# Performance work log

Hardware: AMD Instinct MI355X
Metric: run time of the kernel (lower is better)

Reference implementation:

```python
import jax, jax.numpy as jnp
import numpy as np

N_NODES = 51200
N_EDGES = 614400
ORIG = 92
AFL = 64      # atom_fea_len
NFL = 64      # nbr_fea_len
BINS = 100
N_CONV = 3
EPS = 1e-5


def _bn(h, g, b):
    # BatchNorm1d in training mode: biased batch statistics over dim 0
    mu = h.mean(0)
    var = h.var(0)
    return (h - mu) * jax.lax.rsqrt(var + EPS) * g + b


def setup_inputs() -> dict:
    key = jax.random.key(0)
    ks = jax.random.split(key, 16)
    inp = {
        "x": jax.random.normal(ks[0], (N_NODES, ORIG), dtype=jnp.float32),
        "edge_index": jax.random.randint(ks[1], (2, N_EDGES), 0, N_NODES, dtype=jnp.int32),
        "edge_attr": jax.random.uniform(ks[2], (N_EDGES, 1), dtype=jnp.float32),
        "batchsize": 128,
        # encoder-level params
        "attention": jnp.ones((ORIG,), jnp.float32),
        "emb_W": jax.random.normal(ks[3], (ORIG, AFL), jnp.float32) / np.sqrt(ORIG),
        "emb_b": jnp.zeros((AFL,), jnp.float32),
        # per-conv params stacked along axis 0 (n_conv layers)
        "ad_w1": jax.random.normal(ks[4], (N_CONV, 1, BINS), jnp.float32),
        "ad_b1": jnp.zeros((N_CONV, BINS), jnp.float32),
        "ad_w2": jax.random.normal(ks[5], (N_CONV, BINS, BINS), jnp.float32) / np.sqrt(BINS),
        "ad_b2": jnp.zeros((N_CONV, BINS), jnp.float32),
        "ad_alpha": jax.random.uniform(ks[6], (N_CONV, 1), dtype=jnp.float32),
        "ad_lut": jax.random.uniform(ks[7], (N_CONV, BINS, NFL), dtype=jnp.float32),
        "fc_W": jax.random.normal(ks[8], (N_CONV, 2 * AFL + NFL, 2 * AFL), jnp.float32) / np.sqrt(2 * AFL + NFL),
        "fc_b": jnp.zeros((N_CONV, 2 * AFL), jnp.float32),
        "bn1_g": jnp.ones((N_CONV, 2 * AFL), jnp.float32),
        "bn1_b": jnp.zeros((N_CONV, 2 * AFL), jnp.float32),
        "bn2_g": jnp.ones((N_CONV, AFL), jnp.float32),
        "bn2_b": jnp.zeros((N_CONV, AFL), jnp.float32),
        # pre_pooling linear
        "pp_W": jax.random.normal(ks[9], (AFL, AFL), jnp.float32) / np.sqrt(AFL),
        "pp_b": jnp.zeros((AFL,), jnp.float32),
    }
    return inp


def _cgconv(h, src, dst, edge_attr, w1, b1, w2, b2, alpha, lut, fcW, fcb, g1, be1, g2, be2):
    # AutoDiscretization of the scalar edge feature -> [E, NFL]
    v2 = jax.nn.leaky_relu(edge_attr @ w1 + b1)               # [E, BINS]
    v3 = v2 @ w2 + b2 + alpha * v2                            # [E, BINS]
    e = jax.nn.softmax(v3, axis=-1) @ lut                     # [E, NFL]
    # message: gather endpoints, fused gated MLP (x_i = target, x_j = source)
    z = jnp.concatenate([h[dst], h[src], e], axis=1) @ fcW + fcb  # [E, 2*AFL]
    z = _bn(z, g1, be1)
    nbr_filter, nbr_core = jnp.split(z, 2, axis=1)
    msg = jax.nn.relu(nbr_filter) * jax.nn.relu(nbr_core)     # [E, AFL]
    # aggregate (scatter-add to target nodes) + update
    aggr = jax.ops.segment_sum(msg, dst, num_segments=N_NODES)
    return jax.nn.relu(h + _bn(aggr, g2, be2))


def reference(x, edge_index, edge_attr, batchsize, attention, emb_W, emb_b,
              ad_w1, ad_b1, ad_w2, ad_b2, ad_alpha, ad_lut,
              fc_W, fc_b, bn1_g, bn1_b, bn2_g, bn2_b, pp_W, pp_b):
    src = edge_index[0]  # x_j
    dst = edge_index[1]  # x_i / aggregation target
    num_atom = N_NODES // batchsize

    h = (x * attention) @ emb_W + emb_b                       # [N, AFL]
    feas = [h]
    for l in range(N_CONV):
        h = _cgconv(h, src, dst, edge_attr,
                    ad_w1[l], ad_b1[l], ad_w2[l], ad_b2[l], ad_alpha[l], ad_lut[l],
                    fc_W[l], fc_b[l], bn1_g[l], bn1_b[l], bn2_g[l], bn2_b[l])
        feas.append(h)

    A = jnp.concatenate(feas, axis=0)                         # [(n_conv+1)*N, AFL]
    A = jax.nn.softmax(A @ pp_W + pp_b, axis=1)
    A = A.reshape(N_CONV + 1, batchsize, num_atom, AFL)
    crys_fea = A.sum(axis=0).sum(axis=1)                      # [batchsize, AFL]
    return crys_fea
```

## Files before the change

kernel.cpp:

```cpp
#include <hip/hip_runtime.h>

#define N_NODES 51200
#define N_EDGES 614400
#define ORIG 92
#define AFL 64
#define NFL 64
#define BINS 100
#define NCONV 3
#define BN_EPS 1e-5f
#define NTILES (N_EDGES / 16)
#define NGROUPS (NTILES / 2)

typedef __attribute__((ext_vector_type(8))) short bf8;
typedef __attribute__((ext_vector_type(4))) float f32x4;

__device__ __forceinline__ float bflo(unsigned int u) { return __uint_as_float(u << 16); }
__device__ __forceinline__ float bfhi(unsigned int u) { return __uint_as_float(u & 0xffff0000u); }
__device__ __forceinline__ unsigned int f2bf(float f) {
    unsigned int u = __float_as_uint(f);
    return (u + 0x7fffu + ((u >> 16) & 1u)) >> 16;
}
__device__ __forceinline__ short bfs(float f) { return (short)f2bf(f); }

__global__ __launch_bounds__(256) void hist_kernel(const int* __restrict__ ei,
                                                   int* __restrict__ cnt)
{
    int e = blockIdx.x * 256 + threadIdx.x;
    atomicAdd(&cnt[ei[N_EDGES + e]], 1);
}

__global__ __launch_bounds__(1024) void scan_kernel(int* __restrict__ cnt_cursor,
                                                    int* __restrict__ rowptr)
{
    __shared__ int part[1024];
    const int t = threadIdx.x;
    const int base = t * 50;
    int s = 0;
#pragma unroll 10
    for (int i = 0; i < 50; ++i) s += cnt_cursor[base + i];
    part[t] = s;
    __syncthreads();
    for (int off = 1; off < 1024; off <<= 1) {
        int v = (t >= off) ? part[t - off] : 0;
        __syncthreads();
        part[t] += v;
        __syncthreads();
    }
    int run = (t == 0) ? 0 : part[t - 1];
    for (int i = 0; i < 50; ++i) {
        int c = cnt_cursor[base + i];
        rowptr[base + i] = run;
        cnt_cursor[base + i] = run;
        run += c;
    }
    if (t == 1023) rowptr[N_NODES] = run;
}

__global__ __launch_bounds__(256) void permbuild_kernel(const int* __restrict__ ei,
                                                        int* __restrict__ cursor,
                                                        int* __restrict__ perm)
{
    int e = blockIdx.x * 256 + threadIdx.x;
    int d = ei[N_EDGES + e];
    int pos = atomicAdd(&cursor[d], 1);
    perm[pos] = e;
}

__global__ __launch_bounds__(256) void gather_sorted_kernel(
    const int* __restrict__ perm, const float* __restrict__ ea,
    const int* __restrict__ ei,
    float* __restrict__ ea_s, int* __restrict__ src_s, int* __restrict__ dst_s)
{
    int i = blockIdx.x * 256 + threadIdx.x;
    int e = perm[i];
    ea_s[i] = ea[e];
    src_s[i] = ei[e];
    dst_s[i] = ei[N_EDGES + e];
}

__global__ __launch_bounds__(256) void embed_kernel(
    const float* __restrict__ x, const float* __restrict__ att,
    const float* __restrict__ W, const float* __restrict__ b,
    float* __restrict__ h0, unsigned short* __restrict__ hbf)
{
    const int wave = threadIdx.x >> 6, lane = threadIdx.x & 63;
    const int gw = blockIdx.x * 4 + wave;
    const float bv = b[lane];
    for (int n = gw; n < N_NODES; n += gridDim.x * 4) {
        const float* xr = x + (size_t)n * ORIG;
        float acc = bv;
        for (int k = 0; k < ORIG; ++k)
            acc = fmaf(xr[k] * att[k], W[k * AFL + lane], acc);
        h0[(size_t)n * AFL + lane] = acc;
        hbf[(size_t)n * AFL + lane] = (unsigned short)f2bf(acc);
    }
}

#define SBS 202

__global__ __launch_bounds__(512, 1) void edge_kernel(
    const float* __restrict__ ea_s, const int* __restrict__ src_s,
    const int* __restrict__ dst_s,
    const unsigned short* __restrict__ hbf,
    const float* __restrict__ w1, const float* __restrict__ b1,
    const float* __restrict__ w2, const float* __restrict__ b2,
    const float* __restrict__ alpha_p, const float* __restrict__ lut,
    const float* __restrict__ fcW, const float* __restrict__ fcb,
    short* __restrict__ zo, float* __restrict__ stats)
{
    __shared__ short sW2f[7 * 4 * 64 * 8];
    __shared__ short sLutf[4 * 4 * 64 * 8];
    __shared__ short sFcf[6 * 8 * 64 * 8];
    __shared__ float sW1[128], sB1v[128];
    __shared__ short sBuf[8][16 * SBS];

    const int tid = threadIdx.x;
    for (int i = tid; i < 1792; i += 512) {
        int t = i >> 8, rem = i & 255, s = rem >> 6, le = rem & 63;
        int n = 16 * t + (le & 15);
        int kb = 32 * s + ((le >> 4) << 3);
        short* d = &sW2f[i * 8];
#pragma unroll
        for (int j = 0; j < 8; ++j) {
            int k = kb + j;
            d[j] = bfs((n < BINS && k < BINS) ? w2[k * BINS + n] : 0.f);
        }
    }
    for (int i = tid; i < 1024; i += 512) {
        int t = i >> 8, rem = i & 255, s = rem >> 6, le = rem & 63;
        int n = 16 * t + (le & 15);
        int kb = 32 * s + ((le >> 4) << 3);
        short* d = &sLutf[i * 8];
#pragma unroll
        for (int j = 0; j < 8; ++j) {
            int k = kb + j;
            d[j] = bfs(k < BINS ? lut[k * NFL + n] : 0.f);
        }
    }
    for (int i = tid; i < 3072; i += 512) {
        int s = i >> 9, rem = i & 511, t = rem >> 6, le = rem & 63;
        int n = 16 * t + (le & 15);
        int kb = 32 * s + ((le >> 4) << 3);
        short* d = &sFcf[i * 8];
#pragma unroll
        for (int j = 0; j < 8; ++j)
            d[j] = bfs(fcW[(kb + j) * 128 + n]);
    }
    if (tid < 128) {
        sW1[tid]  = (tid < BINS) ? w1[tid] : 0.f;
        sB1v[tid] = (tid < BINS) ? b1[tid] : 0.f;
    }
    __syncthreads();

    const int wave = tid >> 6, lane = tid & 63;
    const int ln = lane & 15, q = lane >> 4;
    short* sB = &sBuf[wave][0];
    const float alpha = alpha_p[0];

    float w1c[7], b1c[7], b2c[7];
#pragma unroll
    for (int t = 0; t < 7; ++t) {
        int c = ln + 16 * t;
        bool v = c < BINS;
        w1c[t] = v ? w1[c] : 0.f;
        b1c[t] = v ? b1[c] : 0.f;
        b2c[t] = v ? b2[c] : 0.f;
    }
    float fbias[8];
#pragma unroll
    for (int t = 0; t < 8; ++t) fbias[t] = fcb[ln + 16 * t];

    float ss[8], sq[8];
#pragma unroll
    for (int t = 0; t < 8; ++t) { ss[t] = 0.f; sq[t] = 0.f; }

    int g = blockIdx.x * 8 + wave;
    float avA = 0.f, avB = 0.f;
    int snA = 0, dnA = 0, snB = 0, dnB = 0;
    if (g < NGROUPS) {
        int b0 = g * 32 + ln;
        avA = ea_s[b0];      snA = src_s[b0];      dnA = dst_s[b0];
        avB = ea_s[b0 + 16]; snB = src_s[b0 + 16]; dnB = dst_s[b0 + 16];
    }

    for (; g < NGROUPS; g += 2048) {
        const int ebase = g * 32;
        bf8 acA[6], acB[6];
        acA[0] = *(const bf8*)&hbf[(size_t)dnA * 64 + 8 * q];
        acA[1] = *(const bf8*)&hbf[(size_t)dnA * 64 + 32 + 8 * q];
        acA[2] = *(const bf8*)&hbf[(size_t)snA * 64 + 8 * q];
        acA[3] = *(const bf8*)&hbf[(size_t)snA * 64 + 32 + 8 * q];
        acB[0] = *(const bf8*)&hbf[(size_t)dnB * 64 + 8 * q];
        acB[1] = *(const bf8*)&hbf[(size_t)dnB * 64 + 32 + 8 * q];
        acB[2] = *(const bf8*)&hbf[(size_t)snB * 64 + 8 * q];
        acB[3] = *(const bf8*)&hbf[(size_t)snB * 64 + 32 + 8 * q];
        const int gn = g + 2048;
        const int gs = (gn < NGROUPS) ? gn : g;
        const int bN = gs * 32 + ln;
        float avAN = ea_s[bN];      int snAN = src_s[bN];      int dnAN = dst_s[bN];
        float avBN = ea_s[bN + 16]; int snBN = src_s[bN + 16]; int dnBN = dst_s[bN + 16];

        bf8 aA[4], aB[4];
#pragma unroll
        for (int s = 0; s < 4; ++s) {
            const int kb = 32 * s + 8 * q;
            float4 w0 = *(const float4*)&sW1[kb];
            float4 w4 = *(const float4*)&sW1[kb + 4];
            float4 c0 = *(const float4*)&sB1v[kb];
            float4 c4 = *(const float4*)&sB1v[kb + 4];
            float wk[8] = {w0.x, w0.y, w0.z, w0.w, w4.x, w4.y, w4.z, w4.w};
            float ck[8] = {c0.x, c0.y, c0.z, c0.w, c4.x, c4.y, c4.z, c4.w};
#pragma unroll
            for (int j = 0; j < 8; ++j) {
                float vA = fmaf(avA, wk[j], ck[j]);
                vA = vA > 0.f ? vA : 0.01f * vA;
                aA[s][j] = bfs(vA);
                float vB = fmaf(avB, wk[j], ck[j]);
                vB = vB > 0.f ? vB : 0.01f * vB;
                aB[s][j] = bfs(vB);
            }
        }
        f32x4 accA[7], accB[7];
#pragma unroll
        for (int r = 0; r < 4; ++r) {
            float arA = __shfl(avA, q * 4 + r, 64);
            float arB = __shfl(avB, q * 4 + r, 64);
#pragma unroll
            for (int t = 0; t < 7; ++t) {
                float vA = fmaf(arA, w1c[t], b1c[t]);
                vA = vA > 0.f ? vA : 0.01f * vA;
                accA[t][r] = fmaf(alpha, vA, b2c[t]);
                float vB = fmaf(arB, w1c[t], b1c[t]);
                vB = vB > 0.f ? vB : 0.01f * vB;
                accB[t][r] = fmaf(alpha, vB, b2c[t]);
            }
        }
#pragma unroll
        for (int s = 0; s < 4; ++s)
#pragma unroll
            for (int t = 0; t < 7; ++t) {
                bf8 bw = *(const bf8*)&sW2f[((t * 4 + s) * 64 + lane) * 8];
                accA[t] = __builtin_amdgcn_mfma_f32_16x16x32_bf16(aA[s], bw, accA[t], 0, 0, 0);
                accB[t] = __builtin_amdgcn_mfma_f32_16x16x32_bf16(aB[s], bw, accB[t], 0, 0, 0);
            }
#pragma unroll
        for (int r = 0; r < 4; ++r) {
            float evA[7], evB[7], sumA = 0.f, sumB = 0.f;
#pragma unroll
            for (int t = 0; t < 7; ++t) {
                bool on = (t < 6) || (ln < 4);
                evA[t] = on ? __expf(accA[t][r]) : 0.f; sumA += evA[t];
                evB[t] = on ? __expf(accB[t][r]) : 0.f; sumB += evB[t];
            }
#pragma unroll
            for (int o = 8; o >= 1; o >>= 1) {
                sumA += __shfl_xor(sumA, o, 16);
                sumB += __shfl_xor(sumB, o, 16);
            }
            float iA = 1.0f / sumA, iB = 1.0f / sumB;
#pragma unroll
            for (int t = 0; t < 7; ++t) { accA[t][r] = evA[t] * iA; accB[t][r] = evB[t] * iB; }
        }
#pragma unroll
        for (int i = 0; i < 7; ++i) {
            int idx = i * 64 + lane;
            int row = idx / 28, c = 100 + (idx - row * 28);
            sB[row * SBS + c] = 0;
        }
#pragma unroll
        for (int r = 0; r < 4; ++r)
#pragma unroll
            for (int t = 0; t < 7; ++t)
                if (t < 6 || ln < 4) sB[(q * 4 + r) * SBS + ln + 16 * t] = bfs(accA[t][r]);
        bf8 apA[4];
#pragma unroll
        for (int s = 0; s < 4; ++s) apA[s] = *(const bf8*)&sB[ln * SBS + 32 * s + 8 * q];
#pragma unroll
        for (int r = 0; r < 4; ++r)
#pragma unroll
            for (int t = 0; t < 7; ++t)
                if (t < 6 || ln < 4) sB[(q * 4 + r) * SBS + ln + 16 * t] = bfs(accB[t][r]);
        bf8 apB[4];
#pragma unroll
        for (int s = 0; s < 4; ++s) apB[s] = *(const bf8*)&sB[ln * SBS + 32 * s + 8 * q];
        f32x4 eaccA[4], eaccB[4];
#pragma unroll
        for (int t = 0; t < 4; ++t) {
            eaccA[t] = (f32x4){0.f, 0.f, 0.f, 0.f};
            eaccB[t] = (f32x4){0.f, 0.f, 0.f, 0.f};
        }
#pragma unroll
        for (int s = 0; s < 4; ++s)
#pragma unroll
            for (int t = 0; t < 4; ++t) {
                bf8 bl = *(const bf8*)&sLutf[((t * 4 + s) * 64 + lane) * 8];
                eaccA[t] = __builtin_amdgcn_mfma_f32_16x16x32_bf16(apA[s], bl, eaccA[t], 0, 0, 0);
                eaccB[t] = __builtin_amdgcn_mfma_f32_16x16x32_bf16(apB[s], bl, eaccB[t], 0, 0, 0);
            }
#pragma unroll
        for (int t = 0; t < 4; ++t)
#pragma unroll
            for (int r = 0; r < 4; ++r)
                sB[(q * 4 + r) * SBS + 128 + ln + 16 * t] = bfs(eaccA[t][r]);
        acA[4] = *(const bf8*)&sB[ln * SBS + 128 + 8 * q];
        acA[5] = *(const bf8*)&sB[ln * SBS + 160 + 8 * q];
#pragma unroll
        for (int t = 0; t < 4; ++t)
#pragma unroll
            for (int r = 0; r < 4; ++r)
                sB[(q * 4 + r) * SBS + 128 + ln + 16 * t] = bfs(eaccB[t][r]);
        acB[4] = *(const bf8*)&sB[ln * SBS + 128 + 8 * q];
        acB[5] = *(const bf8*)&sB[ln * SBS + 160 + 8 * q];
        f32x4 zaccA[8], zaccB[8];
#pragma unroll
        for (int t = 0; t < 8; ++t) {
            zaccA[t] = (f32x4){fbias[t], fbias[t], fbias[t], fbias[t]};
            zaccB[t] = (f32x4){fbias[t], fbias[t], fbias[t], fbias[t]};
        }
#pragma unroll
        for (int s = 0; s < 6; ++s)
#pragma unroll
            for (int t = 0; t < 8; ++t) {
                bf8 bw = *(const bf8*)&sFcf[((s * 8 + t) * 64 + lane) * 8];
                zaccA[t] = __builtin_amdgcn_mfma_f32_16x16x32_bf16(acA[s], bw, zaccA[t], 0, 0, 0);
                zaccB[t] = __builtin_amdgcn_mfma_f32_16x16x32_bf16(acB[s], bw, zaccB[t], 0, 0, 0);
            }
#pragma unroll
        for (int t = 0; t < 8; ++t)
#pragma unroll
            for (int r = 0; r < 4; ++r) {
                float zv = zaccA[t][r];
                ss[t] += zv; sq[t] = fmaf(zv, zv, sq[t]);
                sB[(q * 4 + r) * SBS + ln + 16 * t] = bfs(zv);
            }
#pragma unroll
        for (int i = 0; i < 4; ++i) {
            int idx = i * 64 + lane;
            int row = idx >> 4, seg = idx & 15;
            bf8 v = *(const bf8*)&sB[row * SBS + seg * 8];
            *(bf8*)&zo[(size_t)(ebase + row) * 128 + seg * 8] = v;
        }
#pragma unroll
        for (int t = 0; t < 8; ++t)
#pragma unroll
            for (int r = 0; r < 4; ++r) {
                float zv = zaccB[t][r];
                ss[t] += zv; sq[t] = fmaf(zv, zv, sq[t]);
                sB[(q * 4 + r) * SBS + ln + 16 * t] = bfs(zv);
            }
#pragma unroll
        for (int i = 0; i < 4; ++i) {
            int idx = i * 64 + lane;
            int row = idx >> 4, seg = idx & 15;
            bf8 v = *(const bf8*)&sB[row * SBS + seg * 8];
            *(bf8*)&zo[(size_t)(ebase + 16 + row) * 128 + seg * 8] = v;
        }
        avA = avAN; snA = snAN; dnA = dnAN;
        avB = avBN; snB = snBN; dnB = dnBN;
    }

#pragma unroll
    for (int t = 0; t < 8; ++t) {
        ss[t] += __shfl_xor(ss[t], 16, 64); ss[t] += __shfl_xor(ss[t], 32, 64);
        sq[t] += __shfl_xor(sq[t], 16, 64); sq[t] += __shfl_xor(sq[t], 32, 64);
    }
    __syncthreads();
    float* sred = (float*)&sBuf[0][0];
    if (q == 0) {
#pragma unroll
        for (int t = 0; t < 8; ++t) {
            sred[wave * 128 + ln + 16 * t] = ss[t];
            sred[1024 + wave * 128 + ln + 16 * t] = sq[t];
        }
    }
    __syncthreads();
    if (tid < 256) {
        int base = (tid < 128) ? 0 : 1024;
        int col = tid & 127;
        float s = 0.f;
#pragma unroll
        for (int w = 0; w < 8; ++w) s += sred[base + w * 128 + col];
        atomicAdd(&stats[tid], s);
    }
}

__global__ void bn_fin_kernel(const float* __restrict__ stats,
                              const float* __restrict__ g, const float* __restrict__ b,
                              float* __restrict__ bnp, int C, float invN)
{
    int c = threadIdx.x;
    if (c >= C) return;
    float mu = stats[c] * invN;
    float var = stats[C + c] * invN - mu * mu;
    float sc = g[c] * rsqrtf(var + BN_EPS);
    bnp[c] = sc;
    bnp[C + c] = b[c] - mu * sc;
}

__global__ __launch_bounds__(256) void aggregate_kernel(
    const unsigned int* __restrict__ z32, const int* __restrict__ rowptr,
    const float* __restrict__ bnp, float* __restrict__ aggr)
{
    const int n0 = (blockIdx.x * 4 + (threadIdx.x >> 6)) * 2;
    const int lane = threadIdx.x & 63;
    const int f2 = lane & 31, slot = lane >> 5, f = 2 * f2;
    const float sc0 = bnp[f], sc1 = bnp[f + 1];
    const float sh0 = bnp[128 + f], sh1 = bnp[128 + f + 1];
    const float tc0 = bnp[64 + f], tc1 = bnp[64 + f + 1];
    const float th0 = bnp[192 + f], th1 = bnp[192 + f + 1];
    const int s0 = rowptr[n0], m0 = rowptr[n0 + 1], m1 = rowptr[n0 + 2];
    float a0 = 0.f, a1 = 0.f, b0 = 0.f, b1 = 0.f;
    int ea_ = s0 + slot, eb_ = m0 + slot;
    while (ea_ < m0 || eb_ < m1) {
        if (ea_ < m0) {
            unsigned int ua = z32[(size_t)ea_ * 64 + f2];
            unsigned int ub = z32[(size_t)ea_ * 64 + 32 + f2];
            float zf0 = fmaf(bflo(ua), sc0, sh0);
            float zf1 = fmaf(bfhi(ua), sc1, sh1);
            float zc0 = fmaf(bflo(ub), tc0, th0);
            float zc1 = fmaf(bfhi(ub), tc1, th1);
            a0 += fmaxf(zf0, 0.f) * fmaxf(zc0, 0.f);
            a1 += fmaxf(zf1, 0.f) * fmaxf(zc1, 0.f);
        }
        if (eb_ < m1) {
            unsigned int ua = z32[(size_t)eb_ * 64 + f2];
            unsigned int ub = z32[(size_t)eb_ * 64 + 32 + f2];
            float zf0 = fmaf(bflo(ua), sc0, sh0);
            float zf1 = fmaf(bfhi(ua), sc1, sh1);
            float zc0 = fmaf(bflo(ub), tc0, th0);
            float zc1 = fmaf(bfhi(ub), tc1, th1);
            b0 += fmaxf(zf0, 0.f) * fmaxf(zc0, 0.f);
            b1 += fmaxf(zf1, 0.f) * fmaxf(zc1, 0.f);
        }
        ea_ += 2; eb_ += 2;
    }
    a0 += __shfl_xor(a0, 32, 64);
    a1 += __shfl_xor(a1, 32, 64);
    b0 += __shfl_xor(b0, 32, 64);
    b1 += __shfl_xor(b1, 32, 64);
    if (slot == 0) {
        float2 w0; w0.x = a0; w0.y = a1;
        *(float2*)&aggr[(size_t)n0 * 64 + f] = w0;
        float2 w1; w1.x = b0; w1.y = b1;
        *(float2*)&aggr[(size_t)(n0 + 1) * 64 + f] = w1;
    }
}

__global__ __launch_bounds__(256) void colstats64_kernel(
    const float* __restrict__ x, int rows, float* __restrict__ stats)
{
    int f = threadIdx.x & 63, sub = threadIdx.x >> 6;
    float s = 0.f, q = 0.f;
    for (int r = blockIdx.x * 4 + sub; r < rows; r += gridDim.x * 4) {
        float v = x[(size_t)r * 64 + f];
        s += v; q = fmaf(v, v, q);
    }
    __shared__ float ls[4][64], lq[4][64];
    ls[sub][f] = s; lq[sub][f] = q;
    __syncthreads();
    if (sub == 0) {
        s = ls[0][f] + ls[1][f] + ls[2][f] + ls[3][f];
        q = lq[0][f] + lq[1][f] + lq[2][f] + lq[3][f];
        atomicAdd(&stats[f], s);
        atomicAdd(&stats[64 + f], q);
    }
}

__global__ __launch_bounds__(256) void update_kernel(
    const float* __restrict__ h, const float* __restrict__ aggr,
    const float* __restrict__ bnp, float* __restrict__ hout,
    unsigned short* __restrict__ hbf)
{
    int t = blockIdx.x * 256 + threadIdx.x;
    int f = t & 63;
    float v = fmaf(aggr[t], bnp[f], bnp[64 + f]);
    float r = fmaxf(h[t] + v, 0.f);
    hout[t] = r;
    hbf[t] = (unsigned short)f2bf(r);
}

__global__ __launch_bounds__(256) void pool_kernel(
    const float* __restrict__ hbuf, const float* __restrict__ ppW,
    const float* __restrict__ ppb, float* __restrict__ out)
{
    const int l = blockIdx.x >> 7, b = blockIdx.x & 127;
    const int wave = threadIdx.x >> 6, lane = threadIdx.x & 63;
    float wcol[64];
#pragma unroll
    for (int k = 0; k < 64; ++k) wcol[k] = ppW[k * 64 + lane];
    const float bias = ppb[lane];
    const float* base = hbuf + ((size_t)l * N_NODES + (size_t)b * 400) * 64;
    __shared__ float srow[4][2][64];
    __shared__ float sacc[4][64];
    float acc = 0.f;
    for (int r = wave * 2; r < 400; r += 8) {
        srow[wave][0][lane] = base[(size_t)r * 64 + lane];
        srow[wave][1][lane] = base[(size_t)r * 64 + 64 + lane];
        float lg0 = bias, lg1 = bias;
#pragma unroll
        for (int k4 = 0; k4 < 64; k4 += 4) {
            float4 a = *(const float4*)&srow[wave][0][k4];
            float4 c = *(const float4*)&srow[wave][1][k4];
            lg0 = fmaf(a.x, wcol[k4 + 0], lg0); lg1 = fmaf(c.x, wcol[k4 + 0], lg1);
            lg0 = fmaf(a.y, wcol[k4 + 1], lg0); lg1 = fmaf(c.y, wcol[k4 + 1], lg1);
            lg0 = fmaf(a.z, wcol[k4 + 2], lg0); lg1 = fmaf(c.z, wcol[k4 + 2], lg1);
            lg0 = fmaf(a.w, wcol[k4 + 3], lg0); lg1 = fmaf(c.w, wcol[k4 + 3], lg1);
        }
        float m0 = lg0, m1 = lg1;
#pragma unroll
        for (int o = 32; o >= 1; o >>= 1) {
            m0 = fmaxf(m0, __shfl_xor(m0, o, 64));
            m1 = fmaxf(m1, __shfl_xor(m1, o, 64));
        }
        float e0 = __expf(lg0 - m0), e1 = __expf(lg1 - m1);
        float s0 = e0, s1 = e1;
#pragma unroll
        for (int o = 32; o >= 1; o >>= 1) {
            s0 += __shfl_xor(s0, o, 64);
            s1 += __shfl_xor(s1, o, 64);
        }
        acc += e0 * (1.0f / s0) + e1 * (1.0f / s1);
    }
    sacc[wave][lane] = acc;
    __syncthreads();
    if (wave == 0) {
        float t = sacc[0][lane] + sacc[1][lane] + sacc[2][lane] + sacc[3][lane];
        atomicAdd(&out[(size_t)b * 64 + lane], t);
    }
}

extern "C" void kernel_launch(void* const* d_in, const int* in_sizes, int n_in,
                              void* d_out, int out_size, void* d_ws, size_t ws_size,
                              hipStream_t stream)
{
    const float* x        = (const float*)d_in[0];
    const int*   ei       = (const int*)d_in[1];
    const float* ea       = (const float*)d_in[2];
    const float* att      = (const float*)d_in[4];
    const float* embW     = (const float*)d_in[5];
    const float* embB     = (const float*)d_in[6];
    const float* ad_w1    = (const float*)d_in[7];
    const float* ad_b1    = (const float*)d_in[8];
    const float* ad_w2    = (const float*)d_in[9];
    const float* ad_b2    = (const float*)d_in[10];
    const float* ad_alpha = (const float*)d_in[11];
    const float* ad_lut   = (const float*)d_in[12];
    const float* fc_W     = (const float*)d_in[13];
    const float* fc_b     = (const float*)d_in[14];
    const float* bn1_g    = (const float*)d_in[15];
    const float* bn1_b    = (const float*)d_in[16];
    const float* bn2_g    = (const float*)d_in[17];
    const float* bn2_b    = (const float*)d_in[18];
    const float* ppW      = (const float*)d_in[19];
    const float* ppb      = (const float*)d_in[20];
    float* out = (float*)d_out;

    char* ws = (char*)d_ws;
    float* hbuf   = (float*)ws;
    short* zU     = (short*)(ws + 52428800);
    float* aggr   = (float*)(ws + 209715200);
    float* stats1 = (float*)(ws + 222822400);
    float* bnp1   = stats1 + 256;
    float* stats2 = bnp1 + 256;
    float* bnp2   = stats2 + 128;
    int*   rowptr = (int*)(ws + 222826496);
    int*   cursor = (int*)(ws + 223031360);
    float* ea_s   = (float*)(ws + 223236160);
    int*   src_s  = (int*)(ws + 225693760);
    int*   dst_s  = (int*)(ws + 228151360);
    int*   perm   = (int*)(ws + 230608960);
    unsigned short* hbf = (unsigned short*)(ws + 230608960);

    hipMemsetAsync(cursor, 0, N_NODES * sizeof(int), stream);
    hist_kernel<<<N_EDGES / 256, 256, 0, stream>>>(ei, cursor);
    scan_kernel<<<1, 1024, 0, stream>>>(cursor, rowptr);
    permbuild_kernel<<<N_EDGES / 256, 256, 0, stream>>>(ei, cursor, perm);
    gather_sorted_kernel<<<N_EDGES / 256, 256, 0, stream>>>(perm, ea, ei, ea_s, src_s, dst_s);

    hipMemsetAsync(out, 0, 128 * 64 * sizeof(float), stream);
    embed_kernel<<<512, 256, 0, stream>>>(x, att, embW, embB, hbuf, hbf);

    for (int l = 0; l < NCONV; ++l) {
        float* h  = hbuf + (size_t)l * N_NODES * AFL;
        float* hn = h + (size_t)N_NODES * AFL;
        hipMemsetAsync(stats1, 0, 768 * 4, stream);
        edge_kernel<<<256, 512, 0, stream>>>(
            ea_s, src_s, dst_s, hbf,
            ad_w1 + l * BINS, ad_b1 + l * BINS,
            ad_w2 + l * BINS * BINS, ad_b2 + l * BINS,
            ad_alpha + l, ad_lut + l * BINS * NFL,
            fc_W + l * 192 * 128, fc_b + l * 128,
            zU, stats1);
        bn_fin_kernel<<<1, 128, 0, stream>>>(stats1, bn1_g + l * 128, bn1_b + l * 128,
                                             bnp1, 128, 1.0f / N_EDGES);
        aggregate_kernel<<<N_NODES / 8, 256, 0, stream>>>((const unsigned int*)zU, rowptr,
                                                          bnp1, aggr);
        colstats64_kernel<<<256, 256, 0, stream>>>(aggr, N_NODES, stats2);
        bn_fin_kernel<<<1, 128, 0, stream>>>(stats2, bn2_g + l * 64, bn2_b + l * 64,
                                             bnp2, 64, 1.0f / N_NODES);
        update_kernel<<<N_NODES * 64 / 256, 256, 0, stream>>>(h, aggr, bnp2, hn, hbf);
    }

    pool_kernel<<<512, 256, 0, stream>>>(hbuf, ppW, ppb, out);
}
```

Baseline: 1.141 ms.

## Fold LUT into FC weights and fuse BN finalize into consumer kernels

Precomputes M = lut @ fc_W[edge part] once per layer in a small prep kernel. The edge kernel then multiplies the discretization probabilities directly by M, dropping the intermediate LUT matmul, its LDS round trip and one bf16 rounding step. The K dimension of the FC grows from 192 to 256 but the separate 4x4 MFMA stage disappears. The bn_fin launches are removed, and each block of aggregate and update recomputes the BN scale and shift into shared memory, which adds a little redundant per-block work.

```diff
diff --git a/kernel.cpp b/kernel.cpp
--- a/kernel.cpp
+++ b/kernel.cpp
@@ -78,6 +78,30 @@
     dst_s[i] = ei[N_EDGES + e];
 }
 
+__global__ __launch_bounds__(256) void prepM_kernel(
+    const float* __restrict__ ad_lut, const float* __restrict__ fc_W,
+    unsigned short* __restrict__ Mf)
+{
+    int gi = blockIdx.x * 256 + threadIdx.x;
+    int l = gi >> 11;
+    int i = gi & 2047;
+    int s = i >> 9, rem = i & 511, t = rem >> 6, le = rem & 63;
+    int n = 16 * t + (le & 15);
+    int kb = 32 * s + ((le >> 4) << 3);
+    const float* lut  = ad_lut + (size_t)l * BINS * NFL;
+    const float* fcWe = fc_W + (size_t)l * 192 * 128 + 128 * 128;
+    unsigned short* d = Mf + (size_t)l * 16384 + (size_t)i * 8;
+#pragma unroll
+    for (int j = 0; j < 8; ++j) {
+        int k = kb + j;
+        float acc = 0.f;
+        if (k < BINS)
+            for (int j2 = 0; j2 < 64; ++j2)
+                acc = fmaf(lut[k * NFL + j2], fcWe[j2 * 128 + n], acc);
+        d[j] = (unsigned short)f2bf(acc);
+    }
+}
+
 __global__ __launch_bounds__(256) void embed_kernel(
     const float* __restrict__ x, const float* __restrict__ att,
     const float* __restrict__ W, const float* __restrict__ b,
@@ -104,13 +128,13 @@
     const unsigned short* __restrict__ hbf,
     const float* __restrict__ w1, const float* __restrict__ b1,
     const float* __restrict__ w2, const float* __restrict__ b2,
-    const float* __restrict__ alpha_p, const float* __restrict__ lut,
+    const float* __restrict__ alpha_p,
     const float* __restrict__ fcW, const float* __restrict__ fcb,
+    const unsigned short* __restrict__ Mf,
     short* __restrict__ zo, float* __restrict__ stats)
 {
     __shared__ short sW2f[7 * 4 * 64 * 8];
-    __shared__ short sLutf[4 * 4 * 64 * 8];
-    __shared__ short sFcf[6 * 8 * 64 * 8];
+    __shared__ short sZW[8 * 8 * 64 * 8];
     __shared__ float sW1[128], sB1v[128];
     __shared__ short sBuf[8][16 * SBS];
 
@@ -126,26 +150,17 @@
             d[j] = bfs((n < BINS && k < BINS) ? w2[k * BINS + n] : 0.f);
         }
     }
-    for (int i = tid; i < 1024; i += 512) {
-        int t = i >> 8, rem = i & 255, s = rem >> 6, le = rem & 63;
-        int n = 16 * t + (le & 15);
-        int kb = 32 * s + ((le >> 4) << 3);
-        short* d = &sLutf[i * 8];
-#pragma unroll
-        for (int j = 0; j < 8; ++j) {
-            int k = kb + j;
-            d[j] = bfs(k < BINS ? lut[k * NFL + n] : 0.f);
-        }
-    }
-    for (int i = tid; i < 3072; i += 512) {
+    for (int i = tid; i < 2048; i += 512) {
         int s = i >> 9, rem = i & 511, t = rem >> 6, le = rem & 63;
         int n = 16 * t + (le & 15);
         int kb = 32 * s + ((le >> 4) << 3);
-        short* d = &sFcf[i * 8];
+        short* d = &sZW[i * 8];
 #pragma unroll
         for (int j = 0; j < 8; ++j)
             d[j] = bfs(fcW[(kb + j) * 128 + n]);
     }
+    for (int i = tid; i < 2048; i += 512)
+        *(uint4*)&sZW[(2048 + i) * 8] = *(const uint4*)&Mf[(size_t)i * 8];
     if (tid < 128) {
         sW1[tid]  = (tid < BINS) ? w1[tid] : 0.f;
         sB1v[tid] = (tid < BINS) ? b1[tid] : 0.f;
@@ -185,7 +200,7 @@
 
     for (; g < NGROUPS; g += 2048) {
         const int ebase = g * 32;
-        bf8 acA[6], acB[6];
+        bf8 acA[4], acB[4];
         acA[0] = *(const bf8*)&hbf[(size_t)dnA * 64 + 8 * q];
         acA[1] = *(const bf8*)&hbf[(size_t)dnA * 64 + 32 + 8 * q];
         acA[2] = *(const bf8*)&hbf[(size_t)snA * 64 + 8 * q];
@@ -283,34 +298,6 @@
         bf8 apB[4];
 #pragma unroll
         for (int s = 0; s < 4; ++s) apB[s] = *(const bf8*)&sB[ln * SBS + 32 * s + 8 * q];
-        f32x4 eaccA[4], eaccB[4];
-#pragma unroll
-        for (int t = 0; t < 4; ++t) {
-            eaccA[t] = (f32x4){0.f, 0.f, 0.f, 0.f};
-            eaccB[t] = (f32x4){0.f, 0.f, 0.f, 0.f};
-        }
-#pragma unroll
-        for (int s = 0; s < 4; ++s)
-#pragma unroll
-            for (int t = 0; t < 4; ++t) {
-                bf8 bl = *(const bf8*)&sLutf[((t * 4 + s) * 64 + lane) * 8];
-                eaccA[t] = __builtin_amdgcn_mfma_f32_16x16x32_bf16(apA[s], bl, eaccA[t], 0, 0, 0);
-                eaccB[t] = __builtin_amdgcn_mfma_f32_16x16x32_bf16(apB[s], bl, eaccB[t], 0, 0, 0);
-            }
-#pragma unroll
-        for (int t = 0; t < 4; ++t)
-#pragma unroll
-            for (int r = 0; r < 4; ++r)
-                sB[(q * 4 + r) * SBS + 128 + ln + 16 * t] = bfs(eaccA[t][r]);
-        acA[4] = *(const bf8*)&sB[ln * SBS + 128 + 8 * q];
-        acA[5] = *(const bf8*)&sB[ln * SBS + 160 + 8 * q];
-#pragma unroll
-        for (int t = 0; t < 4; ++t)
-#pragma unroll
-            for (int r = 0; r < 4; ++r)
-                sB[(q * 4 + r) * SBS + 128 + ln + 16 * t] = bfs(eaccB[t][r]);
-        acB[4] = *(const bf8*)&sB[ln * SBS + 128 + 8 * q];
-        acB[5] = *(const bf8*)&sB[ln * SBS + 160 + 8 * q];
         f32x4 zaccA[8], zaccB[8];
 #pragma unroll
         for (int t = 0; t < 8; ++t) {
@@ -318,13 +305,16 @@
             zaccB[t] = (f32x4){fbias[t], fbias[t], fbias[t], fbias[t]};
         }
 #pragma unroll
-        for (int s = 0; s < 6; ++s)
+        for (int s = 0; s < 8; ++s) {
+            bf8 aopA = (s < 4) ? acA[s] : apA[s - 4];
+            bf8 aopB = (s < 4) ? acB[s] : apB[s - 4];
 #pragma unroll
             for (int t = 0; t < 8; ++t) {
-                bf8 bw = *(const bf8*)&sFcf[((s * 8 + t) * 64 + lane) * 8];
-                zaccA[t] = __builtin_amdgcn_mfma_f32_16x16x32_bf16(acA[s], bw, zaccA[t], 0, 0, 0);
-                zaccB[t] = __builtin_amdgcn_mfma_f32_16x16x32_bf16(acB[s], bw, zaccB[t], 0, 0, 0);
-            }
+                bf8 bw = *(const bf8*)&sZW[((s * 8 + t) * 64 + lane) * 8];
+                zaccA[t] = __builtin_amdgcn_mfma_f32_16x16x32_bf16(aopA, bw, zaccA[t], 0, 0, 0);
+                zaccB[t] = __builtin_amdgcn_mfma_f32_16x16x32_bf16(aopB, bw, zaccB[t], 0, 0, 0);
+            }
+        }
 #pragma unroll
         for (int t = 0; t < 8; ++t)
 #pragma unroll
@@ -384,23 +374,23 @@
     }
 }
 
-__global__ void bn_fin_kernel(const float* __restrict__ stats,
-                              const float* __restrict__ g, const float* __restrict__ b,
-                              float* __restrict__ bnp, int C, float invN)
-{
-    int c = threadIdx.x;
-    if (c >= C) return;
-    float mu = stats[c] * invN;
-    float var = stats[C + c] * invN - mu * mu;
-    float sc = g[c] * rsqrtf(var + BN_EPS);
-    bnp[c] = sc;
-    bnp[C + c] = b[c] - mu * sc;
-}
-
 __global__ __launch_bounds__(256) void aggregate_kernel(
     const unsigned int* __restrict__ z32, const int* __restrict__ rowptr,
-    const float* __restrict__ bnp, float* __restrict__ aggr)
-{
+    const float* __restrict__ stats1,
+    const float* __restrict__ g1, const float* __restrict__ b1g,
+    float* __restrict__ aggr)
+{
+    __shared__ float bnp[256];
+    if (threadIdx.x < 128) {
+        int c = threadIdx.x;
+        float mu = stats1[c] * (1.0f / N_EDGES);
+        float var = stats1[128 + c] * (1.0f / N_EDGES) - mu * mu;
+        float sc = g1[c] * rsqrtf(var + BN_EPS);
+        bnp[c] = sc;
+        bnp[128 + c] = b1g[c] - mu * sc;
+    }
+    __syncthreads();
+
     const int n0 = (blockIdx.x * 4 + (threadIdx.x >> 6)) * 2;
     const int lane = threadIdx.x & 63;
     const int f2 = lane & 31, slot = lane >> 5, f = 2 * f2;
@@ -468,9 +458,20 @@
 
 __global__ __launch_bounds__(256) void update_kernel(
     const float* __restrict__ h, const float* __restrict__ aggr,
-    const float* __restrict__ bnp, float* __restrict__ hout,
-    unsigned short* __restrict__ hbf)
-{
+    const float* __restrict__ stats2,
+    const float* __restrict__ g2, const float* __restrict__ b2g,
+    float* __restrict__ hout, unsigned short* __restrict__ hbf)
+{
+    __shared__ float bnp[128];
+    if (threadIdx.x < 64) {
+        int c = threadIdx.x;
+        float mu = stats2[c] * (1.0f / N_NODES);
+        float var = stats2[64 + c] * (1.0f / N_NODES) - mu * mu;
+        float sc = g2[c] * rsqrtf(var + BN_EPS);
+        bnp[c] = sc;
+        bnp[64 + c] = b2g[c] - mu * sc;
+    }
+    __syncthreads();
     int t = blockIdx.x * 256 + threadIdx.x;
     int f = t & 63;
     float v = fmaf(aggr[t], bnp[f], bnp[64 + f]);
@@ -560,9 +561,7 @@
     short* zU     = (short*)(ws + 52428800);
     float* aggr   = (float*)(ws + 209715200);
     float* stats1 = (float*)(ws + 222822400);
-    float* bnp1   = stats1 + 256;
-    float* stats2 = bnp1 + 256;
-    float* bnp2   = stats2 + 128;
+    float* stats2 = stats1 + 256;
     int*   rowptr = (int*)(ws + 222826496);
     int*   cursor = (int*)(ws + 223031360);
     float* ea_s   = (float*)(ws + 223236160);
@@ -570,6 +569,7 @@
     int*   dst_s  = (int*)(ws + 228151360);
     int*   perm   = (int*)(ws + 230608960);
     unsigned short* hbf = (unsigned short*)(ws + 230608960);
+    unsigned short* Mf  = (unsigned short*)(ws + 237162560);
 
     hipMemsetAsync(cursor, 0, N_NODES * sizeof(int), stream);
     hist_kernel<<<N_EDGES / 256, 256, 0, stream>>>(ei, cursor);
@@ -577,28 +577,29 @@
     permbuild_kernel<<<N_EDGES / 256, 256, 0, stream>>>(ei, cursor, perm);
     gather_sorted_kernel<<<N_EDGES / 256, 256, 0, stream>>>(perm, ea, ei, ea_s, src_s, dst_s);
 
+    prepM_kernel<<<24, 256, 0, stream>>>(ad_lut, fc_W, Mf);
     hipMemsetAsync(out, 0, 128 * 64 * sizeof(float), stream);
     embed_kernel<<<512, 256, 0, stream>>>(x, att, embW, embB, hbuf, hbf);
 
     for (int l = 0; l < NCONV; ++l) {
         float* h  = hbuf + (size_t)l * N_NODES * AFL;
         float* hn = h + (size_t)N_NODES * AFL;
-        hipMemsetAsync(stats1, 0, 768 * 4, stream);
+        hipMemsetAsync(stats1, 0, 384 * 4, stream);
         edge_kernel<<<256, 512, 0, stream>>>(
             ea_s, src_s, dst_s, hbf,
             ad_w1 + l * BINS, ad_b1 + l * BINS,
             ad_w2 + l * BINS * BINS, ad_b2 + l * BINS,
-            ad_alpha + l, ad_lut + l * BINS * NFL,
+            ad_alpha + l,
             fc_W + l * 192 * 128, fc_b + l * 128,
+            Mf + (size_t)l * 16384,
             zU, stats1);
-        bn_fin_kernel<<<1, 128, 0, stream>>>(stats1, bn1_g + l * 128, bn1_b + l * 128,
-                                             bnp1, 128, 1.0f / N_EDGES);
         aggregate_kernel<<<N_NODES / 8, 256, 0, stream>>>((const unsigned int*)zU, rowptr,
-                                                          bnp1, aggr);
+                                                          stats1, bn1_g + l * 128, bn1_b + l * 128,
+                                                          aggr);
         colstats64_kernel<<<256, 256, 0, stream>>>(aggr, N_NODES, stats2);
-        bn_fin_kernel<<<1, 128, 0, stream>>>(stats2, bn2_g + l * 64, bn2_b + l * 64,
-                                             bnp2, 64, 1.0f / N_NODES);
-        update_kernel<<<N_NODES * 64 / 256, 256, 0, stream>>>(h, aggr, bnp2, hn, hbf);
+        update_kernel<<<N_NODES * 64 / 256, 256, 0, stream>>>(h, aggr, stats2,
+                                                              bn2_g + l * 64, bn2_b + l * 64,
+                                                              hn, hbf);
     }
 
     pool_kernel<<<512, 256, 0, stream>>>(hbuf, ppW, ppb, out);
```

After: 1.116 ms. 2.2% less time.
